# Performance work log

Hardware: AMD Instinct MI355X
Metric: run time of the kernel (lower is better)

The kernel has to match this reference:

```python
import jax, jax.numpy as jnp
import numpy as np

N, A, B, C = 256, 1024, 64, 16


def setup_inputs() -> dict:
    key = jax.random.key(0)
    k1, k2, k3 = jax.random.split(key, 3)
    x = jax.random.normal(k1, (N, A), dtype=jnp.float32)
    weight = jax.random.normal(k2, (A, B * C), dtype=jnp.float32) * 0.02
    bias = jax.random.normal(k3, (B,), dtype=jnp.float32) * 0.02
    return {"x": x, "weight": weight, "bias": bias}


def reference(x, weight, bias):
    # x: [N, A]; weight: [A, B*C]; bias: [B]
    n = x.shape[0]
    mat = (x @ weight).reshape(n, B, C)              # [N, B, C]
    # pairwise L1 over the C (kernel) axis -> [N, N, B]
    l1 = jnp.abs(mat[:, None, :, :] - mat[None, :, :, :]).sum(axis=-1)
    # exp(-L1), sum over the first (broadcast) axis as in the torch code,
    # which includes the self term exp(0)=1
    out = jnp.exp(-l1).sum(axis=0) + bias            # [N, B]
    return out
```

## Files before the change

kernel.cpp:

```cpp
#include <hip/hip_runtime.h>

#define LOG2E 1.4426950408889634f

typedef __bf16 bf16x8 __attribute__((ext_vector_type(8)));
typedef float  f32x4  __attribute__((ext_vector_type(4)));

__device__ inline unsigned short f2bf(float f){
  unsigned u = __float_as_uint(f);
  unsigned r = u + 0x7FFFu + ((u >> 16) & 1u);
  return (unsigned short)(r >> 16);
}

__global__ __launch_bounds__(256) void k_cvt_x(const float* __restrict__ x,
                                               unsigned short* __restrict__ xb){
  int t = blockIdx.x * 256 + threadIdx.x;
  const float4* x4 = (const float4*)x;
  float4 a = x4[t * 2], b = x4[t * 2 + 1];
  uint4 o;
  o.x = f2bf(a.x) | ((unsigned)f2bf(a.y) << 16);
  o.y = f2bf(a.z) | ((unsigned)f2bf(a.w) << 16);
  o.z = f2bf(b.x) | ((unsigned)f2bf(b.y) << 16);
  o.w = f2bf(b.z) | ((unsigned)f2bf(b.w) << 16);
  ((uint4*)xb)[t] = o;
}

__global__ __launch_bounds__(256) void k_tr_w(const float* __restrict__ W,
                                              unsigned short* __restrict__ Wt){
  __shared__ unsigned short T[64 * 72];
  int kt = blockIdx.x * 64, nt = blockIdx.y * 64;
  int t = threadIdx.x;
  int col4 = t & 15;
  int g = t >> 4;
  #pragma unroll
  for (int s = 0; s < 2; ++s){
    int k0 = 2 * (g + 16 * s);
    float4 a = *((const float4*)(W + (size_t)(kt + k0    ) * 1024 + nt) + col4);
    float4 b = *((const float4*)(W + (size_t)(kt + k0 + 1) * 1024 + nt) + col4);
    *(unsigned*)(&T[(col4*4+0)*72 + k0]) = f2bf(a.x) | ((unsigned)f2bf(b.x) << 16);
    *(unsigned*)(&T[(col4*4+1)*72 + k0]) = f2bf(a.y) | ((unsigned)f2bf(b.y) << 16);
    *(unsigned*)(&T[(col4*4+2)*72 + k0]) = f2bf(a.z) | ((unsigned)f2bf(b.z) << 16);
    *(unsigned*)(&T[(col4*4+3)*72 + k0]) = f2bf(a.w) | ((unsigned)f2bf(b.w) << 16);
  }
  __syncthreads();
  int nl = t >> 2;
  int kq = t & 3;
  uint4* dst = (uint4*)(Wt + (size_t)(nt + nl) * 1024 + kt + kq * 16);
  const uint4* src = (const uint4*)(&T[nl * 72 + kq * 16]);
  dst[0] = src[0];
  dst[1] = src[1];
}

__global__ __launch_bounds__(256) void k_gemm(const unsigned short* __restrict__ A,
                                              const unsigned short* __restrict__ Bt,
                                              float* __restrict__ C){
  __shared__ unsigned short As[64 * 72];
  __shared__ unsigned short Bs[64 * 72];
  int m0 = blockIdx.x * 64, n0 = blockIdx.y * 64;
  int t = threadIdx.x;
  int lane = t & 63, w = t >> 6;
  int wrow = (w & 1) * 32, wcol = (w >> 1) * 32;
  int r16  = lane & 15;
  int quad = lane >> 4;

  f32x4 acc[2][2];
  #pragma unroll
  for (int p = 0; p < 2; ++p)
    #pragma unroll
    for (int q = 0; q < 2; ++q)
      #pragma unroll
      for (int e = 0; e < 4; ++e) acc[p][q][e] = 0.f;

  for (int kt = 0; kt < 1024; kt += 64){
    #pragma unroll
    for (int q = t; q < 512; q += 256){
      int row = q >> 3, c8 = q & 7;
      *(uint4*)(&As[row * 72 + c8 * 8]) = *(const uint4*)(A  + (size_t)(m0 + row) * 1024 + kt + c8 * 8);
      *(uint4*)(&Bs[row * 72 + c8 * 8]) = *(const uint4*)(Bt + (size_t)(n0 + row) * 1024 + kt + c8 * 8);
    }
    __syncthreads();
    #pragma unroll
    for (int kk = 0; kk < 2; ++kk){
      int ko = kk * 32 + quad * 8;
      bf16x8 a0 = *(const bf16x8*)(&As[(wrow      + r16) * 72 + ko]);
      bf16x8 a1 = *(const bf16x8*)(&As[(wrow + 16 + r16) * 72 + ko]);
      bf16x8 b0 = *(const bf16x8*)(&Bs[(wcol      + r16) * 72 + ko]);
      bf16x8 b1 = *(const bf16x8*)(&Bs[(wcol + 16 + r16) * 72 + ko]);
      acc[0][0] = __builtin_amdgcn_mfma_f32_16x16x32_bf16(a0, b0, acc[0][0], 0, 0, 0);
      acc[0][1] = __builtin_amdgcn_mfma_f32_16x16x32_bf16(a0, b1, acc[0][1], 0, 0, 0);
      acc[1][0] = __builtin_amdgcn_mfma_f32_16x16x32_bf16(a1, b0, acc[1][0], 0, 0, 0);
      acc[1][1] = __builtin_amdgcn_mfma_f32_16x16x32_bf16(a1, b1, acc[1][1], 0, 0, 0);
    }
    __syncthreads();
  }
  #pragma unroll
  for (int p = 0; p < 2; ++p)
    #pragma unroll
    for (int q = 0; q < 2; ++q)
      #pragma unroll
      for (int r = 0; r < 4; ++r){
        int row = m0 + wrow + p * 16 + quad * 4 + r;
        int col = n0 + wcol + q * 16 + r16;
        C[(size_t)row * 1024 + col] = acc[p][q][r];
      }
}

__global__ __launch_bounds__(512) void k_pair(const float* __restrict__ mat,
                                              const float* __restrict__ bias,
                                              float* __restrict__ out){
  __shared__ float red[8][64];
  int b  = blockIdx.x >> 2;
  int jc = blockIdx.x & 3;
  int t = threadIdx.x;
  int lane = t & 63, w = t >> 6;
  int j = jc * 64 + lane;

  const float* jr = mat + (size_t)j * 1024 + b * 16;
  float oj[16];
  #pragma unroll
  for (int c4 = 0; c4 < 4; ++c4){
    float4 v = *(const float4*)(jr + c4 * 4);
    oj[c4*4+0] = v.x * LOG2E; oj[c4*4+1] = v.y * LOG2E;
    oj[c4*4+2] = v.z * LOG2E; oj[c4*4+3] = v.w * LOG2E;
  }
  int i0 = w * 32 + (lane & 31);
  const float* ir = mat + (size_t)i0 * 1024 + b * 16;
  float oi[16];
  #pragma unroll
  for (int c4 = 0; c4 < 4; ++c4){
    float4 v = *(const float4*)(ir + c4 * 4);
    oi[c4*4+0] = v.x * LOG2E; oi[c4*4+1] = v.y * LOG2E;
    oi[c4*4+2] = v.z * LOG2E; oi[c4*4+3] = v.w * LOG2E;
  }

  float acc = 0.f;
  for (int ii = 0; ii < 32; ++ii){
    float p0 = 0.f, p1 = 0.f, p2 = 0.f, p3 = 0.f;
    #pragma unroll
    for (int c = 0; c < 16; c += 4){
      float b0 = __uint_as_float(__builtin_amdgcn_readlane(__float_as_uint(oi[c+0]), ii));
      float b1 = __uint_as_float(__builtin_amdgcn_readlane(__float_as_uint(oi[c+1]), ii));
      float b2 = __uint_as_float(__builtin_amdgcn_readlane(__float_as_uint(oi[c+2]), ii));
      float b3 = __uint_as_float(__builtin_amdgcn_readlane(__float_as_uint(oi[c+3]), ii));
      p0 += fabsf(oj[c+0] - b0);
      p1 += fabsf(oj[c+1] - b1);
      p2 += fabsf(oj[c+2] - b2);
      p3 += fabsf(oj[c+3] - b3);
    }
    acc += exp2f(-((p0 + p1) + (p2 + p3)));
  }
  red[w][lane] = acc;
  __syncthreads();
  if (w == 0){
    float tot = 0.f;
    #pragma unroll
    for (int ww = 0; ww < 8; ++ww) tot += red[ww][lane];
    out[(size_t)j * 64 + b] = tot + bias[b];
  }
}

extern "C" void kernel_launch(void* const* d_in, const int* in_sizes, int n_in,
                              void* d_out, int out_size, void* d_ws, size_t ws_size,
                              hipStream_t stream){
  const float* x    = (const float*)d_in[0];
  const float* W    = (const float*)d_in[1];
  const float* bias = (const float*)d_in[2];
  float* out = (float*)d_out;

  unsigned short* xb  = (unsigned short*)d_ws;
  unsigned short* Wt  = xb + 256 * 1024;
  float*          mat = (float*)(Wt + 1024 * 1024);

  k_cvt_x<<<128, 256, 0, stream>>>(x, xb);
  k_tr_w<<<dim3(16, 16), 256, 0, stream>>>(W, Wt);
  k_gemm<<<dim3(4, 16), 256, 0, stream>>>(xb, Wt, mat);
  k_pair<<<256, 512, 0, stream>>>(mat, bias, out);
}
```

Before: 90.70 us.

## Fuse bf16 conversion and weight transpose into GEMM, stage pair rows in LDS

Removes the separate x-conversion and W-transpose kernels. The GEMM now reads fp32 inputs directly, converts them to bf16 in registers, and writes them into LDS, with an XOR swizzle on the transposed B tile. It also register-prefetches the next K tile so the global loads overlap with the MFMA work. The pair kernel now loads all 256 rows for a band into shared memory and reads i-rows from LDS instead of broadcasting with readlane. This cuts two launches and an intermediate round trip through memory, but the GEMM grid stays small (64 blocks), so each block re-reads and re-converts its fp32 inputs.

```diff
diff --git a/kernel.cpp b/kernel.cpp
--- a/kernel.cpp
+++ b/kernel.cpp
@@ -10,57 +10,25 @@
   unsigned r = u + 0x7FFFu + ((u >> 16) & 1u);
   return (unsigned short)(r >> 16);
 }
-
-__global__ __launch_bounds__(256) void k_cvt_x(const float* __restrict__ x,
-                                               unsigned short* __restrict__ xb){
-  int t = blockIdx.x * 256 + threadIdx.x;
-  const float4* x4 = (const float4*)x;
-  float4 a = x4[t * 2], b = x4[t * 2 + 1];
-  uint4 o;
-  o.x = f2bf(a.x) | ((unsigned)f2bf(a.y) << 16);
-  o.y = f2bf(a.z) | ((unsigned)f2bf(a.w) << 16);
-  o.z = f2bf(b.x) | ((unsigned)f2bf(b.y) << 16);
-  o.w = f2bf(b.z) | ((unsigned)f2bf(b.w) << 16);
-  ((uint4*)xb)[t] = o;
+__device__ inline unsigned pack2(float lo, float hi){
+  return (unsigned)f2bf(lo) | ((unsigned)f2bf(hi) << 16);
 }
 
-__global__ __launch_bounds__(256) void k_tr_w(const float* __restrict__ W,
-                                              unsigned short* __restrict__ Wt){
-  __shared__ unsigned short T[64 * 72];
-  int kt = blockIdx.x * 64, nt = blockIdx.y * 64;
-  int t = threadIdx.x;
-  int col4 = t & 15;
-  int g = t >> 4;
-  #pragma unroll
-  for (int s = 0; s < 2; ++s){
-    int k0 = 2 * (g + 16 * s);
-    float4 a = *((const float4*)(W + (size_t)(kt + k0    ) * 1024 + nt) + col4);
-    float4 b = *((const float4*)(W + (size_t)(kt + k0 + 1) * 1024 + nt) + col4);
-    *(unsigned*)(&T[(col4*4+0)*72 + k0]) = f2bf(a.x) | ((unsigned)f2bf(b.x) << 16);
-    *(unsigned*)(&T[(col4*4+1)*72 + k0]) = f2bf(a.y) | ((unsigned)f2bf(b.y) << 16);
-    *(unsigned*)(&T[(col4*4+2)*72 + k0]) = f2bf(a.z) | ((unsigned)f2bf(b.z) << 16);
-    *(unsigned*)(&T[(col4*4+3)*72 + k0]) = f2bf(a.w) | ((unsigned)f2bf(b.w) << 16);
-  }
-  __syncthreads();
-  int nl = t >> 2;
-  int kq = t & 3;
-  uint4* dst = (uint4*)(Wt + (size_t)(nt + nl) * 1024 + kt + kq * 16);
-  const uint4* src = (const uint4*)(&T[nl * 72 + kq * 16]);
-  dst[0] = src[0];
-  dst[1] = src[1];
-}
-
-__global__ __launch_bounds__(256) void k_gemm(const unsigned short* __restrict__ A,
-                                              const unsigned short* __restrict__ Bt,
-                                              float* __restrict__ C){
+__global__ __launch_bounds__(256) void k_gemm_fused(const float* __restrict__ X,
+                                                    const float* __restrict__ Wm,
+                                                    float* __restrict__ mat){
   __shared__ unsigned short As[64 * 72];
   __shared__ unsigned short Bs[64 * 72];
-  int m0 = blockIdx.x * 64, n0 = blockIdx.y * 64;
-  int t = threadIdx.x;
-  int lane = t & 63, w = t >> 6;
-  int wrow = (w & 1) * 32, wcol = (w >> 1) * 32;
-  int r16  = lane & 15;
-  int quad = lane >> 4;
+  const int m0 = blockIdx.x * 64, n0 = blockIdx.y * 64;
+  const int t = threadIdx.x;
+  const int lane = t & 63, w = t >> 6;
+  const int wrow = (w & 1) * 32, wcol = (w >> 1) * 32;
+  const int r16 = lane & 15, quad = lane >> 4;
+
+  const int ar = t >> 2, aq = t & 3;
+  const int bc = t & 15, bg = t >> 4;
+  const float* ap = X + (size_t)(m0 + ar) * 1024 + aq * 16;
+  const float* bp = Wm + n0 + bc * 4;
 
   f32x4 acc[2][2];
   #pragma unroll
@@ -70,27 +38,56 @@
       #pragma unroll
       for (int e = 0; e < 4; ++e) acc[p][q][e] = 0.f;
 
+  float4 pa[4], pb[4];
+  #pragma unroll
+  for (int r = 0; r < 4; ++r) pa[r] = *(const float4*)(ap + r * 4);
+  #pragma unroll
+  for (int r = 0; r < 4; ++r) pb[r] = *(const float4*)(bp + (size_t)(4 * bg + r) * 1024);
+
   for (int kt = 0; kt < 1024; kt += 64){
-    #pragma unroll
-    for (int q = t; q < 512; q += 256){
-      int row = q >> 3, c8 = q & 7;
-      *(uint4*)(&As[row * 72 + c8 * 8]) = *(const uint4*)(A  + (size_t)(m0 + row) * 1024 + kt + c8 * 8);
-      *(uint4*)(&Bs[row * 72 + c8 * 8]) = *(const uint4*)(Bt + (size_t)(n0 + row) * 1024 + kt + c8 * 8);
+    __syncthreads();
+    {
+      unsigned short* d = &As[ar * 72 + aq * 16];
+      uint4 o;
+      o.x = pack2(pa[0].x, pa[0].y); o.y = pack2(pa[0].z, pa[0].w);
+      o.z = pack2(pa[1].x, pa[1].y); o.w = pack2(pa[1].z, pa[1].w);
+      *(uint4*)d = o;
+      o.x = pack2(pa[2].x, pa[2].y); o.y = pack2(pa[2].z, pa[2].w);
+      o.z = pack2(pa[3].x, pa[3].y); o.w = pack2(pa[3].z, pa[3].w);
+      *(uint4*)(d + 8) = o;
+    }
+    {
+      #pragma unroll
+      for (int e = 0; e < 4; ++e){
+        const int n = bc * 4 + e;
+        uint2 o;
+        o.x = pack2(((const float*)&pb[0])[e], ((const float*)&pb[1])[e]);
+        o.y = pack2(((const float*)&pb[2])[e], ((const float*)&pb[3])[e]);
+        const int cw = (bg >> 1) ^ ((n >> 3) & 7);
+        *(uint2*)(&Bs[n * 72 + cw * 8 + (bg & 1) * 4]) = o;
+      }
     }
     __syncthreads();
+    if (kt + 64 < 1024){
+      #pragma unroll
+      for (int r = 0; r < 4; ++r) pa[r] = *(const float4*)(ap + kt + 64 + r * 4);
+      #pragma unroll
+      for (int r = 0; r < 4; ++r) pb[r] = *(const float4*)(bp + (size_t)(kt + 64 + 4 * bg + r) * 1024);
+    }
     #pragma unroll
     for (int kk = 0; kk < 2; ++kk){
-      int ko = kk * 32 + quad * 8;
+      const int ko = kk * 32 + quad * 8;
       bf16x8 a0 = *(const bf16x8*)(&As[(wrow      + r16) * 72 + ko]);
       bf16x8 a1 = *(const bf16x8*)(&As[(wrow + 16 + r16) * 72 + ko]);
-      bf16x8 b0 = *(const bf16x8*)(&Bs[(wcol      + r16) * 72 + ko]);
-      bf16x8 b1 = *(const bf16x8*)(&Bs[(wcol + 16 + r16) * 72 + ko]);
+      const int c = kk * 4 + quad;
+      const int nb0 = wcol + r16, nb1 = wcol + 16 + r16;
+      bf16x8 b0 = *(const bf16x8*)(&Bs[nb0 * 72 + ((c ^ ((nb0 >> 3) & 7)) * 8)]);
+      bf16x8 b1 = *(const bf16x8*)(&Bs[nb1 * 72 + ((c ^ ((nb1 >> 3) & 7)) * 8)]);
       acc[0][0] = __builtin_amdgcn_mfma_f32_16x16x32_bf16(a0, b0, acc[0][0], 0, 0, 0);
       acc[0][1] = __builtin_amdgcn_mfma_f32_16x16x32_bf16(a0, b1, acc[0][1], 0, 0, 0);
       acc[1][0] = __builtin_amdgcn_mfma_f32_16x16x32_bf16(a1, b0, acc[1][0], 0, 0, 0);
       acc[1][1] = __builtin_amdgcn_mfma_f32_16x16x32_bf16(a1, b1, acc[1][1], 0, 0, 0);
     }
-    __syncthreads();
   }
   #pragma unroll
   for (int p = 0; p < 2; ++p)
@@ -98,55 +95,51 @@
     for (int q = 0; q < 2; ++q)
       #pragma unroll
       for (int r = 0; r < 4; ++r){
-        int row = m0 + wrow + p * 16 + quad * 4 + r;
-        int col = n0 + wcol + q * 16 + r16;
-        C[(size_t)row * 1024 + col] = acc[p][q][r];
+        const int row = m0 + wrow + p * 16 + quad * 4 + r;
+        const int col = n0 + wcol + q * 16 + r16;
+        mat[(size_t)row * 1024 + col] = acc[p][q][r];
       }
 }
 
 __global__ __launch_bounds__(512) void k_pair(const float* __restrict__ mat,
                                               const float* __restrict__ bias,
                                               float* __restrict__ out){
+  __shared__ float L[256 * 16];
   __shared__ float red[8][64];
-  int b  = blockIdx.x >> 2;
-  int jc = blockIdx.x & 3;
-  int t = threadIdx.x;
-  int lane = t & 63, w = t >> 6;
-  int j = jc * 64 + lane;
+  const int b = blockIdx.x >> 2, jc = blockIdx.x & 3;
+  const int t = threadIdx.x, lane = t & 63, w = t >> 6;
 
-  const float* jr = mat + (size_t)j * 1024 + b * 16;
+  #pragma unroll
+  for (int p = 0; p < 2; ++p){
+    const int f = t + p * 512;
+    const int i = f >> 2, q = f & 3;
+    *(float4*)(&L[i * 16 + q * 4]) =
+        *(const float4*)(mat + (size_t)i * 1024 + b * 16 + q * 4);
+  }
+  __syncthreads();
+
+  const int j = jc * 64 + lane;
   float oj[16];
   #pragma unroll
-  for (int c4 = 0; c4 < 4; ++c4){
-    float4 v = *(const float4*)(jr + c4 * 4);
-    oj[c4*4+0] = v.x * LOG2E; oj[c4*4+1] = v.y * LOG2E;
-    oj[c4*4+2] = v.z * LOG2E; oj[c4*4+3] = v.w * LOG2E;
-  }
-  int i0 = w * 32 + (lane & 31);
-  const float* ir = mat + (size_t)i0 * 1024 + b * 16;
-  float oi[16];
-  #pragma unroll
-  for (int c4 = 0; c4 < 4; ++c4){
-    float4 v = *(const float4*)(ir + c4 * 4);
-    oi[c4*4+0] = v.x * LOG2E; oi[c4*4+1] = v.y * LOG2E;
-    oi[c4*4+2] = v.z * LOG2E; oi[c4*4+3] = v.w * LOG2E;
+  for (int q = 0; q < 4; ++q){
+    float4 v = *(const float4*)(&L[j * 16 + q * 4]);
+    oj[q*4+0] = v.x; oj[q*4+1] = v.y; oj[q*4+2] = v.z; oj[q*4+3] = v.w;
   }
 
   float acc = 0.f;
-  for (int ii = 0; ii < 32; ++ii){
-    float p0 = 0.f, p1 = 0.f, p2 = 0.f, p3 = 0.f;
-    #pragma unroll
-    for (int c = 0; c < 16; c += 4){
-      float b0 = __uint_as_float(__builtin_amdgcn_readlane(__float_as_uint(oi[c+0]), ii));
-      float b1 = __uint_as_float(__builtin_amdgcn_readlane(__float_as_uint(oi[c+1]), ii));
-      float b2 = __uint_as_float(__builtin_amdgcn_readlane(__float_as_uint(oi[c+2]), ii));
-      float b3 = __uint_as_float(__builtin_amdgcn_readlane(__float_as_uint(oi[c+3]), ii));
-      p0 += fabsf(oj[c+0] - b0);
-      p1 += fabsf(oj[c+1] - b1);
-      p2 += fabsf(oj[c+2] - b2);
-      p3 += fabsf(oj[c+3] - b3);
-    }
-    acc += exp2f(-((p0 + p1) + (p2 + p3)));
+  const int i0 = w * 32;
+  for (int ii = i0; ii < i0 + 32; ++ii){
+    const float4* fr = (const float4*)(&L[ii * 16]);
+    float4 f0 = fr[0], f1 = fr[1], f2 = fr[2], f3 = fr[3];
+    float p0 = fabsf(oj[0]  - f0.x) + fabsf(oj[1]  - f0.y)
+             + fabsf(oj[2]  - f0.z) + fabsf(oj[3]  - f0.w);
+    float p1 = fabsf(oj[4]  - f1.x) + fabsf(oj[5]  - f1.y)
+             + fabsf(oj[6]  - f1.z) + fabsf(oj[7]  - f1.w);
+    float p2 = fabsf(oj[8]  - f2.x) + fabsf(oj[9]  - f2.y)
+             + fabsf(oj[10] - f2.z) + fabsf(oj[11] - f2.w);
+    float p3 = fabsf(oj[12] - f3.x) + fabsf(oj[13] - f3.y)
+             + fabsf(oj[14] - f3.z) + fabsf(oj[15] - f3.w);
+    acc += exp2f(-LOG2E * ((p0 + p1) + (p2 + p3)));
   }
   red[w][lane] = acc;
   __syncthreads();
@@ -165,13 +158,8 @@
   const float* W    = (const float*)d_in[1];
   const float* bias = (const float*)d_in[2];
   float* out = (float*)d_out;
+  float* mat = (float*)d_ws;
 
-  unsigned short* xb  = (unsigned short*)d_ws;
-  unsigned short* Wt  = xb + 256 * 1024;
-  float*          mat = (float*)(Wt + 1024 * 1024);
-
-  k_cvt_x<<<128, 256, 0, stream>>>(x, xb);
-  k_tr_w<<<dim3(16, 16), 256, 0, stream>>>(W, Wt);
-  k_gemm<<<dim3(4, 16), 256, 0, stream>>>(xb, Wt, mat);
+  k_gemm_fused<<<dim3(4, 16), 256, 0, stream>>>(x, W, mat);
   k_pair<<<256, 512, 0, stream>>>(mat, bias, out);
 }
```

Result: faster. 83.35 us (-8.1%).
